# Kernel optimization log

Hardware: AMD Instinct MI355X
Metric: run time of the kernel (lower is better)

## Reference

```python
import jax, jax.numpy as jnp
import numpy as np

N = 50000      # num vertices
M = 10000      # num hyperedges
NNZ = 1600000  # incidence list length (avg degree 32)
D = 128        # in_features == out_features


def setup_inputs() -> dict:
    key = jax.random.key(0)
    k0, k1, k2, k3, k4, k5 = jax.random.split(key, 6)
    X = jax.random.normal(k0, (N, D), dtype=jnp.float32)
    X0 = jax.random.normal(k1, (N, D), dtype=jnp.float32)
    vertex = jax.random.randint(k2, (NNZ,), 0, N)
    edges = jax.random.randint(k3, (NNZ,), 0, M)
    # nn.Linear(D, D, bias=False) weight, kaiming-uniform-ish scale
    W = jax.random.uniform(k4, (D, D), dtype=jnp.float32,
                           minval=-1.0, maxval=1.0) / np.float32(np.sqrt(D))
    alpha = jax.random.uniform(k5, (), dtype=jnp.float32)
    beta = jnp.float32(0.5)
    return {"X": X, "X0": X0, "W": W, "alpha": alpha, "beta": beta,
            "vertex": vertex, "edges": edges}


def _scatter_mean(vals, idx, num_segments):
    # segment mean; empty segments -> 0 (matches torch_scatter 'mean')
    s = jax.ops.segment_sum(vals, idx, num_segments=num_segments)
    cnt = jax.ops.segment_sum(jnp.ones(idx.shape, vals.dtype), idx,
                              num_segments=num_segments)
    return s / jnp.maximum(cnt, 1.0)[:, None]


def reference(X, X0, W, alpha, beta, vertex, edges):
    Xve = X[vertex]                          # [NNZ, D] gather vertex -> incidence
    Xe = _scatter_mean(Xve, edges, M)        # [M, D]   hyperedge features
    Xev = Xe[edges]                          # [NNZ, D] gather edge -> incidence
    Xv = _scatter_mean(Xev, vertex, N)       # [N, D]   back to vertices
    Xi = (1.0 - alpha) * Xv + alpha * X0     # initial-residual mix
    return (1.0 - beta) * Xi + beta * (Xi @ W.T)  # identity-map mix + linear
```

## Files before the change

### kernel.cpp

```cpp
#include <hip/hip_runtime.h>
#include <hip/hip_bf16.h>


#define DD 128
#define NV 50000
#define ME 10000

#define CHUNK 4096
#define NEB 157
#define NVB 196
#define PB_CAP 12288

typedef __hip_bfloat16 bf16;
typedef __attribute__((ext_vector_type(8))) short short8v;
typedef __attribute__((ext_vector_type(4))) float float4v;

#define OFF_XE    0
#define OFF_ELIST 2560000
#define OFF_VLIST 8960000
#define OFF_EPAIR 15360000
#define OFF_VPAIR 21760000
#define OFF_XB    15360000
#define OFF_VOFF  28160000
#define OFF_EOFF  28360064
#define OFF_CBH   28400128
#define OFF_GBE   28401664
#define OFF_GBV   28402304
#define OFF_GCE   28403136
#define OFF_GCV   28403776
#define OFF_FLAG  28404608
#define OFF_WF    28404624
#define WS_USED   28470160

__device__ __forceinline__ float bf2f(unsigned short s) {
    union { unsigned u; float f; } x; x.u = ((unsigned)s) << 16; return x.f;
}
__device__ __forceinline__ unsigned f2bfu(float x) {
    union { bf16 h; unsigned short u; } c; c.h = __float2bfloat16(x); return (unsigned)c.u;
}
__device__ __forceinline__ float loadf(const void* p, long long i, unsigned f32) {
    if (f32) return ((const float*)p)[i];
    return bf2f(((const unsigned short*)p)[i]);
}
__device__ __forceinline__ float u2f_lo(unsigned x) {
    union { unsigned u; float f; } c; c.u = x << 16; return c.f;
}
__device__ __forceinline__ float u2f_hi(unsigned x) {
    union { unsigned u; float f; } c; c.u = x & 0xFFFF0000u; return c.f;
}
__device__ __forceinline__ void acc8(const uint4& u, float* a) {
    a[0] += u2f_lo(u.x); a[1] += u2f_hi(u.x);
    a[2] += u2f_lo(u.y); a[3] += u2f_hi(u.y);
    a[4] += u2f_lo(u.z); a[5] += u2f_hi(u.z);
    a[6] += u2f_lo(u.w); a[7] += u2f_hi(u.w);
}

__device__ __forceinline__ unsigned wave_is_fp32(const unsigned short* p) {
    int l = threadIdx.x & 63;
    int big = 0;
    for (int i = l; i < 256; i += 64) {
        unsigned e = (p[i] >> 7) & 0xFFu;
        if (e >= 0x90u) big++;
    }
    for (int s = 32; s > 0; s >>= 1) big += __shfl_down(big, s);
    return (__shfl(big, 0) >= 4) ? 1u : 0u;
}

__global__ __launch_bounds__(256) void prep_all(const void* X, const void* X0, const void* W,
                                                const void* beta_p,
                                                const int* __restrict__ vertex,
                                                const int* __restrict__ edges,
                                                unsigned* __restrict__ flags,
                                                unsigned short* __restrict__ Wfrag,
                                                unsigned* __restrict__ cbh, int nnz) {
    __shared__ unsigned h[NEB + NVB];
    int b = blockIdx.x, t = threadIdx.x;

    if (b == 0) {
        if (t < 64) {
            const unsigned short* px[3] = {(const unsigned short*)X,
                                           (const unsigned short*)X0,
                                           (const unsigned short*)W};
            for (int k = 0; k < 3; k++) {
                int big = 0;
                for (int i = t; i < 256; i += 64) {
                    unsigned e = (px[k][i] >> 7) & 0xFFu;
                    if (e >= 0x90u) big++;
                }
                for (int s = 32; s > 0; s >>= 1) big += __shfl_down(big, s);
                if (t == 0) flags[k] = (big >= 4) ? 1u : 0u;
            }
            if (t == 0) {
                unsigned short bb = *(const unsigned short*)beta_p;
                flags[3] = (bb == 0x3F00u) ? 0u : 1u;
            }
        }
        return;
    }

    if (b <= 8) {
        int blob = (b - 1) * 256 + t;
        unsigned fW = wave_is_fp32((const unsigned short*)W);
        unsigned short bu = *(const unsigned short*)beta_p;
        unsigned fS = (bu == 0x3F00u) ? 0u : 1u;
        int lane = blob & 63, kk = (blob >> 6) & 3, ct = blob >> 8;
        int nn = lane & 15, quad = lane >> 4;
        int c = ct * 16 + nn;
        int kbase = kk * 32 + quad * 8;
        float beta = loadf(beta_p, 0, fS);
        float omb = 1.f - beta;
        unsigned short hi[8], lo[8];
#pragma unroll
        for (int j = 0; j < 8; j++) {
            float wv = loadf(W, (long long)c * DD + kbase + j, fW);
            float v = beta * wv + ((kbase + j) == c ? omb : 0.f);
            unsigned short hh = (unsigned short)f2bfu(v);
            hi[j] = hh;
            lo[j] = (unsigned short)f2bfu(v - bf2f(hh));
        }
        uint4 ph, pl;
        ph.x = (unsigned)hi[0] | ((unsigned)hi[1] << 16);
        ph.y = (unsigned)hi[2] | ((unsigned)hi[3] << 16);
        ph.z = (unsigned)hi[4] | ((unsigned)hi[5] << 16);
        ph.w = (unsigned)hi[6] | ((unsigned)hi[7] << 16);
        pl.x = (unsigned)lo[0] | ((unsigned)lo[1] << 16);
        pl.y = (unsigned)lo[2] | ((unsigned)lo[3] << 16);
        pl.z = (unsigned)lo[4] | ((unsigned)lo[5] << 16);
        pl.w = (unsigned)lo[6] | ((unsigned)lo[7] << 16);
        ((uint4*)Wfrag)[blob] = ph;
        ((uint4*)Wfrag)[2048 + blob] = pl;
        return;
    }

    int hb = b - 9;
    for (int i = t; i < NEB + NVB; i += 256) h[i] = 0;
    __syncthreads();
    int stride = 512 * 256;
    for (int i = hb * 256 + t; i < nnz; i += stride) {
        atomicAdd(&h[edges[i] >> 6], 1u);
        atomicAdd(&h[NEB + (vertex[i] >> 8)], 1u);
    }
    __syncthreads();
    for (int i = t; i < NEB + NVB; i += 256) {
        unsigned v = h[i];
        if (v) atomicAdd(&cbh[i], v);
    }
}

__global__ __launch_bounds__(256) void conv_x(const void* __restrict__ X,
                                              unsigned short* __restrict__ Xb,
                                              const unsigned* __restrict__ flags) {
    if (!flags[0]) return;
    int i = blockIdx.x * 256 + threadIdx.x;
    if (i >= NV * DD / 8) return;
    const float4* p = (const float4*)X + (size_t)i * 2;
    float4 a = p[0], b = p[1];
    uint4 o;
    o.x = f2bfu(a.x) | (f2bfu(a.y) << 16);
    o.y = f2bfu(a.z) | (f2bfu(a.w) << 16);
    o.z = f2bfu(b.x) | (f2bfu(b.y) << 16);
    o.w = f2bfu(b.z) | (f2bfu(b.w) << 16);
    ((uint4*)Xb)[i] = o;
}

__global__ void scan353(const unsigned* __restrict__ cbh,
                        unsigned* __restrict__ gbe, unsigned* __restrict__ gbv,
                        unsigned* __restrict__ gce, unsigned* __restrict__ gcv,
                        unsigned* __restrict__ voff, unsigned* __restrict__ eoff,
                        int nnz) {
    __shared__ unsigned s[512];
    int t = threadIdx.x;
    unsigned v = (t < NEB + NVB) ? cbh[t] : 0u;
    s[t] = v;
    __syncthreads();
    for (int st = 1; st < 512; st <<= 1) {
        unsigned u = (t >= st) ? s[t - st] : 0u;
        __syncthreads();
        s[t] += u;
        __syncthreads();
    }
    unsigned excl = s[t] - v;
    if (t < NEB) {
        gbe[t] = excl; gce[t] = excl;
    } else if (t < NEB + NVB) {
        unsigned base = s[NEB - 1];
        gbv[t - NEB] = excl - base;
        gcv[t - NEB] = excl - base;
    }
    if (t == 0) {
        gbe[NEB] = (unsigned)nnz;
        gbv[NVB] = (unsigned)nnz;
        eoff[ME] = (unsigned)nnz;
        voff[NV] = (unsigned)nnz;
    }
}

__global__ __launch_bounds__(256) void build_pairs(const int* __restrict__ vertex,
                                                   const int* __restrict__ edges,
                                                   unsigned* __restrict__ gcur_e,
                                                   unsigned* __restrict__ gcur_v,
                                                   unsigned* __restrict__ epairs,
                                                   unsigned* __restrict__ vpairs, int nnz) {
    __shared__ unsigned buf[CHUNK];
    __shared__ unsigned hist[256], scn[256], loff[256], cur[256], gbase[256];
    int t = threadIdx.x;
    int base = blockIdx.x * CHUNK;
    int len = min(CHUNK, nnz - base);
    if (len <= 0) return;

    for (int phase = 0; phase < 2; phase++) {
        int sh = phase ? 8 : 6;
        int nb = phase ? NVB : NEB;
        unsigned* gcur = phase ? gcur_v : gcur_e;
        unsigned* pairs = phase ? vpairs : epairs;
        if (phase) __syncthreads();
        hist[t] = 0;
        __syncthreads();
        for (int i = t; i < len; i += 256) {
            int key = phase ? vertex[base + i] : edges[base + i];
            atomicAdd(&hist[key >> sh], 1u);
        }
        __syncthreads();
        unsigned hv = hist[t];
        scn[t] = hv;
        __syncthreads();
        for (int st = 1; st < 256; st <<= 1) {
            unsigned u = (t >= st) ? scn[t - st] : 0u;
            __syncthreads();
            scn[t] += u;
            __syncthreads();
        }
        loff[t] = scn[t] - hv;
        cur[t] = scn[t] - hv;
        if (t < nb && hv > 0) gbase[t] = atomicAdd(&gcur[t], hv);
        __syncthreads();
        for (int i = t; i < len; i += 256) {
            int k = phase ? vertex[base + i] : edges[base + i];
            int v2 = phase ? edges[base + i] : vertex[base + i];
            unsigned pk = ((unsigned)k << 16) | (unsigned)v2;
            unsigned p = atomicAdd(&cur[k >> sh], 1u);
            buf[p] = pk;
        }
        __syncthreads();
        for (int i = t; i < len; i += 256) {
            unsigned pk = buf[i];
            unsigned b = (pk >> 16) >> sh;
            pairs[gbase[b] + (i - loff[b])] = pk;
        }
    }
}

__global__ __launch_bounds__(256) void build_lists(const unsigned* __restrict__ epairs,
                                                   const unsigned* __restrict__ vpairs,
                                                   const unsigned* __restrict__ gbe,
                                                   const unsigned* __restrict__ gbv,
                                                   unsigned* __restrict__ eoff,
                                                   unsigned* __restrict__ voff,
                                                   unsigned* __restrict__ elist,
                                                   unsigned* __restrict__ vlist) {
    __shared__ unsigned buf[PB_CAP];
    __shared__ unsigned offs[256], curs[256];
    int b = blockIdx.x, t = threadIdx.x;
    const unsigned* pairs;
    unsigned* off;
    unsigned* list;
    unsigned s0, s1;
    int k0, nk;
    if (b < NEB) {
        pairs = epairs; off = eoff; list = elist;
        k0 = b << 6; nk = min(64, ME - k0);
        s0 = gbe[b]; s1 = gbe[b + 1];
    } else {
        int bb = b - NEB;
        pairs = vpairs; off = voff; list = vlist;
        k0 = bb << 8; nk = min(256, NV - k0);
        s0 = gbv[bb]; s1 = gbv[bb + 1];
    }
    int len = (int)(s1 - s0);

    curs[t] = 0;
    __syncthreads();
    for (int i = t; i < len; i += 256) {
        unsigned pk = pairs[s0 + i];
        atomicAdd(&curs[(pk >> 16) - k0], 1u);
    }
    __syncthreads();
    unsigned hv = curs[t];
    offs[t] = hv;
    __syncthreads();
    for (int st = 1; st < 256; st <<= 1) {
        unsigned u = (t >= st) ? offs[t - st] : 0u;
        __syncthreads();
        offs[t] += u;
        __syncthreads();
    }
    unsigned my_excl = offs[t] - hv;
    __syncthreads();
    offs[t] = my_excl;
    curs[t] = 0;
    if (t < nk) off[k0 + t] = s0 + my_excl;
    __syncthreads();

    if (len <= PB_CAP) {
        for (int i = t; i < len; i += 256) {
            unsigned pk = pairs[s0 + i];
            int lk = (int)(pk >> 16) - k0;
            unsigned p = offs[lk] + atomicAdd(&curs[lk], 1u);
            buf[p] = pk & 0xFFFFu;
        }
        __syncthreads();
        for (int i = t; i < len; i += 256) list[s0 + i] = buf[i];
    } else {
        for (int i = t; i < len; i += 256) {
            unsigned pk = pairs[s0 + i];
            int lk = (int)(pk >> 16) - k0;
            unsigned p = offs[lk] + atomicAdd(&curs[lk], 1u);
            list[s0 + p] = pk & 0xFFFFu;
        }
    }
}

__global__ __launch_bounds__(256, 8) void edge_agg(const void* __restrict__ X,
                                                   const unsigned short* __restrict__ Xb,
                                                   const unsigned* __restrict__ eoff,
                                                   const unsigned* __restrict__ elist,
                                                   unsigned short* __restrict__ Xe,
                                                   const unsigned* __restrict__ flags, int m) {
    __shared__ float red[4][DD];
    int e = blockIdx.x;
    int t = threadIdx.x, lane = t & 63, w = t >> 6;
    const unsigned short* Xp = flags[0] ? Xb : (const unsigned short*)X;
    unsigned s0 = eoff[e], s1 = eoff[e + 1];
    float a[8];
#pragma unroll
    for (int i = 0; i < 8; i++) a[i] = 0.f;

    int sub = t & 15;
    unsigned q = s0 + (unsigned)(t >> 4);
    for (; q + 48 < s1; q += 64) {
        unsigned v0 = elist[q], v1 = elist[q + 16];
        unsigned v2 = elist[q + 32], v3 = elist[q + 48];
        uint4 u0 = *(const uint4*)(Xp + (size_t)v0 * DD + 8 * sub);
        uint4 u1 = *(const uint4*)(Xp + (size_t)v1 * DD + 8 * sub);
        uint4 u2 = *(const uint4*)(Xp + (size_t)v2 * DD + 8 * sub);
        uint4 u3 = *(const uint4*)(Xp + (size_t)v3 * DD + 8 * sub);
        acc8(u0, a); acc8(u1, a); acc8(u2, a); acc8(u3, a);
    }
    for (; q + 16 < s1; q += 32) {
        unsigned v0 = elist[q], v1 = elist[q + 16];
        uint4 u0 = *(const uint4*)(Xp + (size_t)v0 * DD + 8 * sub);
        uint4 u1 = *(const uint4*)(Xp + (size_t)v1 * DD + 8 * sub);
        acc8(u0, a); acc8(u1, a);
    }
    if (q < s1) {
        unsigned v0 = elist[q];
        uint4 u0 = *(const uint4*)(Xp + (size_t)v0 * DD + 8 * sub);
        acc8(u0, a);
    }
#pragma unroll
    for (int i = 0; i < 8; i++) {
        a[i] += __shfl_xor(a[i], 16);
        a[i] += __shfl_xor(a[i], 32);
    }
    if ((lane >> 4) == 0) {
#pragma unroll
        for (int i = 0; i < 8; i++) red[w][8 * sub + i] = a[i];
    }
    __syncthreads();
    if (t < DD) {
        float inv = (s1 > s0) ? 1.f / (float)(s1 - s0) : 1.f;
        float v = (red[0][t] + red[1][t] + red[2][t] + red[3][t]) * inv;
        Xe[(size_t)e * DD + t] = (unsigned short)f2bfu(v);
    }
}

__global__ __launch_bounds__(512, 6) void vertex_out(const unsigned short* __restrict__ Xe,
                                                     const unsigned* __restrict__ voff,
                                                     const unsigned* __restrict__ vlist,
                                                     const void* __restrict__ X0,
                                                     const unsigned short* __restrict__ Wfrag,
                                                     const void* __restrict__ alpha_p,
                                                     void* __restrict__ out,
                                                     const unsigned* __restrict__ flags, int n) {
    __shared__ short8v A_hi[544];
    __shared__ short8v A_lo[544];
    int t = threadIdx.x, lane = t & 63, w = t >> 6;
    unsigned fX = flags[0], f0 = flags[1], fS = flags[3];
    float alpha = loadf(alpha_p, 0, fS);
    float oma = 1.f - alpha;
    int v0 = blockIdx.x * 32;

    int g = lane >> 4, sub = lane & 15;
    for (int j = 0; j < 4; j++) {
        int r = w * 4 + j, v = v0 + r;
        int rt = r >> 4, mm = r & 15;
        int idx = (rt * 4 + (sub >> 2)) * 68 + (sub & 3) * 17 + mm;
        float a[8];
#pragma unroll
        for (int i = 0; i < 8; i++) a[i] = 0.f;
        if (v < n) {
            unsigned s0 = voff[v], s1 = voff[v + 1];
            unsigned q = s0;
            for (; q + 8 <= s1; q += 8) {
                unsigned e0 = vlist[q + g];
                unsigned e1 = vlist[q + 4 + g];
                uint4 u0 = *(const uint4*)(Xe + (size_t)e0 * DD + 8 * sub);
                uint4 u1 = *(const uint4*)(Xe + (size_t)e1 * DD + 8 * sub);
                acc8(u0, a); acc8(u1, a);
            }
            if (q + 4 <= s1) {
                unsigned e0 = vlist[q + g];
                uint4 u0 = *(const uint4*)(Xe + (size_t)e0 * DD + 8 * sub);
                acc8(u0, a);
                q += 4;
            }
            int rem = (int)(s1 - q);
            if (g < rem) {
                unsigned e0 = vlist[q + g];
                uint4 u0 = *(const uint4*)(Xe + (size_t)e0 * DD + 8 * sub);
                acc8(u0, a);
            }
#pragma unroll
            for (int i = 0; i < 8; i++) {
                a[i] += __shfl_xor(a[i], 16);
                a[i] += __shfl_xor(a[i], 32);
            }
            if (g == 0) {
                float inv = (s1 > s0) ? 1.f / (float)(s1 - s0) : 1.f;
                float x0[8];
                if (!f0) {
                    uint4 xu = *(const uint4*)((const unsigned short*)X0 + (size_t)v * DD + 8 * sub);
                    x0[0] = u2f_lo(xu.x); x0[1] = u2f_hi(xu.x);
                    x0[2] = u2f_lo(xu.y); x0[3] = u2f_hi(xu.y);
                    x0[4] = u2f_lo(xu.z); x0[5] = u2f_hi(xu.z);
                    x0[6] = u2f_lo(xu.w); x0[7] = u2f_hi(xu.w);
                } else {
                    const float4* p = (const float4*)((const float*)X0 + (size_t)v * DD + 8 * sub);
                    float4 xA = p[0], xB = p[1];
                    x0[0] = xA.x; x0[1] = xA.y; x0[2] = xA.z; x0[3] = xA.w;
                    x0[4] = xB.x; x0[5] = xB.y; x0[6] = xB.z; x0[7] = xB.w;
                }
                short8v ah, al;
#pragma unroll
                for (int i = 0; i < 8; i++) {
                    float xi = oma * (a[i] * inv) + alpha * x0[i];
                    unsigned short hh = (unsigned short)f2bfu(xi);
                    ah[i] = (short)hh;
                    al[i] = (short)f2bfu(xi - bf2f(hh));
                }
                A_hi[idx] = ah;
                A_lo[idx] = al;
            }
        } else if (g == 0) {
            short8v zf = {0, 0, 0, 0, 0, 0, 0, 0};
            A_hi[idx] = zf;
            A_lo[idx] = zf;
        }
    }

    __syncthreads();
    int rt = w & 1, ct = w >> 1;
    short8v ah[4], al[4];
#pragma unroll
    for (int kk = 0; kk < 4; kk++) {
        int ridx = (rt * 4 + kk) * 68 + (lane >> 4) * 17 + (lane & 15);
        ah[kk] = A_hi[ridx];
        al[kk] = A_lo[ridx];
    }
    const short8v* Bh = (const short8v*)Wfrag;
    const short8v* Bl = Bh + 2048;
#pragma unroll
    for (int tt = 0; tt < 2; tt++) {
        int c2 = ct + 4 * tt;
        float4v acc = {0.f, 0.f, 0.f, 0.f};
#pragma unroll
        for (int kk = 0; kk < 4; kk++) {
            short8v bh = Bh[(c2 * 4 + kk) * 64 + lane];
            short8v bl = Bl[(c2 * 4 + kk) * 64 + lane];
            acc = __builtin_amdgcn_mfma_f32_16x16x32_bf16(ah[kk], bh, acc, 0, 0, 0);
            acc = __builtin_amdgcn_mfma_f32_16x16x32_bf16(al[kk], bh, acc, 0, 0, 0);
            acc = __builtin_amdgcn_mfma_f32_16x16x32_bf16(ah[kk], bl, acc, 0, 0, 0);
        }
        int col = c2 * 16 + (lane & 15);
        int rbase = v0 + rt * 16 + (lane >> 4) * 4;
#pragma unroll
        for (int reg = 0; reg < 4; reg++) {
            int row = rbase + reg;
            if (row < n) {
                if (fX) ((float*)out)[(size_t)row * DD + col] = acc[reg];
                else    ((bf16*)out)[(size_t)row * DD + col] = __float2bfloat16(acc[reg]);
            }
        }
    }
}

extern "C" void kernel_launch(void* const* d_in, const int* in_sizes, int n_in,
                              void* d_out, int out_size, void* d_ws, size_t ws_size,
                              hipStream_t stream) {
    const void* X      = d_in[0];
    const void* X0     = d_in[1];
    const void* W      = d_in[2];
    const void* alpha  = d_in[3];
    const void* beta   = d_in[4];
    const int*  vertex = (const int*)d_in[5];
    const int*  edges  = (const int*)d_in[6];
    const int nnz = in_sizes[5];

    char* ws = (char*)d_ws;
    unsigned short* Xe = (unsigned short*)(ws + OFF_XE);
    unsigned* elist  = (unsigned*)(ws + OFF_ELIST);
    unsigned* vlist  = (unsigned*)(ws + OFF_VLIST);
    unsigned* epairs = (unsigned*)(ws + OFF_EPAIR);
    unsigned* vpairs = (unsigned*)(ws + OFF_VPAIR);
    unsigned short* Xb = (unsigned short*)(ws + OFF_XB);
    unsigned* voff   = (unsigned*)(ws + OFF_VOFF);
    unsigned* eoff   = (unsigned*)(ws + OFF_EOFF);
    unsigned* cbh    = (unsigned*)(ws + OFF_CBH);
    unsigned* gbe    = (unsigned*)(ws + OFF_GBE);
    unsigned* gbv    = (unsigned*)(ws + OFF_GBV);
    unsigned* gce    = (unsigned*)(ws + OFF_GCE);
    unsigned* gcv    = (unsigned*)(ws + OFF_GCV);
    unsigned* flags  = (unsigned*)(ws + OFF_FLAG);
    unsigned short* Wfrag = (unsigned short*)(ws + OFF_WF);

    hipMemsetAsync(ws + OFF_CBH, 0, 1536, stream);

    prep_all<<<521, 256, 0, stream>>>(X, X0, W, beta, vertex, edges,
                                      flags, Wfrag, cbh, nnz);

    scan353<<<1, 512, 0, stream>>>(cbh, gbe, gbv, gce, gcv, voff, eoff, nnz);

    int pa_blocks = (nnz + CHUNK - 1) / CHUNK;
    build_pairs<<<pa_blocks, 256, 0, stream>>>(vertex, edges, gce, gcv,
                                               epairs, vpairs, nnz);

    build_lists<<<NEB + NVB, 256, 0, stream>>>(epairs, vpairs, gbe, gbv,
                                               eoff, voff, elist, vlist);

    conv_x<<<(NV * DD / 8 + 255) / 256, 256, 0, stream>>>(X, Xb, flags);

    edge_agg<<<ME, 256, 0, stream>>>(X, Xb, eoff, elist, Xe, flags, ME);

    vertex_out<<<(NV + 31) / 32, 512, 0, stream>>>(Xe, voff, vlist, X0, Wfrag,
                                                   alpha, d_out, flags, NV);
}
```

Baseline: 269.6 us.

## Reuse edge-sorted buffer for vertex bucketing and shrink vertex_out blocks to 16 rows

build_pairs now reads vertex/edges once into registers and builds the vertex-keyed pass by swapping halves of the edge-sorted packed pairs already held in shared memory. This removes the second global read of the index arrays. vertex_out drops from 32 rows and 512 threads per block to 16 rows and 256 threads, with four waves each covering two column tiles. The smaller blocks give finer scheduling granularity and a smaller LDS footprint, at the cost of loading W fragments from global twice as often per output row.

```diff
diff --git a/kernel.cpp b/kernel.cpp
--- a/kernel.cpp
+++ b/kernel.cpp
@@ -208,45 +208,92 @@
     int len = min(CHUNK, nnz - base);
     if (len <= 0) return;
 
-    for (int phase = 0; phase < 2; phase++) {
-        int sh = phase ? 8 : 6;
-        int nb = phase ? NVB : NEB;
-        unsigned* gcur = phase ? gcur_v : gcur_e;
-        unsigned* pairs = phase ? vpairs : epairs;
-        if (phase) __syncthreads();
-        hist[t] = 0;
-        __syncthreads();
-        for (int i = t; i < len; i += 256) {
-            int key = phase ? vertex[base + i] : edges[base + i];
-            atomicAdd(&hist[key >> sh], 1u);
-        }
-        __syncthreads();
-        unsigned hv = hist[t];
-        scn[t] = hv;
-        __syncthreads();
-        for (int st = 1; st < 256; st <<= 1) {
-            unsigned u = (t >= st) ? scn[t - st] : 0u;
-            __syncthreads();
-            scn[t] += u;
-            __syncthreads();
-        }
-        loff[t] = scn[t] - hv;
-        cur[t] = scn[t] - hv;
-        if (t < nb && hv > 0) gbase[t] = atomicAdd(&gcur[t], hv);
-        __syncthreads();
-        for (int i = t; i < len; i += 256) {
-            int k = phase ? vertex[base + i] : edges[base + i];
-            int v2 = phase ? edges[base + i] : vertex[base + i];
-            unsigned pk = ((unsigned)k << 16) | (unsigned)v2;
-            unsigned p = atomicAdd(&cur[k >> sh], 1u);
+    unsigned pkr[16];
+
+    hist[t] = 0;
+    __syncthreads();
+#pragma unroll
+    for (int it = 0; it < 16; it++) {
+        int i = t + it * 256;
+        if (i < len) {
+            unsigned e = (unsigned)edges[base + i];
+            unsigned v = (unsigned)vertex[base + i];
+            unsigned pk = (e << 16) | v;
+            pkr[it] = pk;
+            atomicAdd(&hist[pk >> 22], 1u);
+        }
+    }
+    __syncthreads();
+    unsigned hv = hist[t];
+    scn[t] = hv;
+    __syncthreads();
+    for (int st = 1; st < 256; st <<= 1) {
+        unsigned u = (t >= st) ? scn[t - st] : 0u;
+        __syncthreads();
+        scn[t] += u;
+        __syncthreads();
+    }
+    loff[t] = scn[t] - hv;
+    cur[t] = scn[t] - hv;
+    if (t < NEB && hv > 0) gbase[t] = atomicAdd(&gcur_e[t], hv);
+    __syncthreads();
+#pragma unroll
+    for (int it = 0; it < 16; it++) {
+        int i = t + it * 256;
+        if (i < len) {
+            unsigned pk = pkr[it];
+            unsigned p = atomicAdd(&cur[pk >> 22], 1u);
             buf[p] = pk;
         }
-        __syncthreads();
-        for (int i = t; i < len; i += 256) {
+    }
+    __syncthreads();
+    for (int i = t; i < len; i += 256) {
+        unsigned pk = buf[i];
+        unsigned b = pk >> 22;
+        epairs[gbase[b] + (i - loff[b])] = pk;
+    }
+
+    __syncthreads();
+    hist[t] = 0;
+    __syncthreads();
+#pragma unroll
+    for (int it = 0; it < 16; it++) {
+        int i = t + it * 256;
+        if (i < len) {
             unsigned pk = buf[i];
-            unsigned b = (pk >> 16) >> sh;
-            pairs[gbase[b] + (i - loff[b])] = pk;
-        }
+            unsigned npk = (pk << 16) | (pk >> 16);
+            pkr[it] = npk;
+            atomicAdd(&hist[npk >> 24], 1u);
+        }
+    }
+    __syncthreads();
+    hv = hist[t];
+    scn[t] = hv;
+    __syncthreads();
+    for (int st = 1; st < 256; st <<= 1) {
+        unsigned u = (t >= st) ? scn[t - st] : 0u;
+        __syncthreads();
+        scn[t] += u;
+        __syncthreads();
+    }
+    loff[t] = scn[t] - hv;
+    cur[t] = scn[t] - hv;
+    if (t < NVB && hv > 0) gbase[t] = atomicAdd(&gcur_v[t], hv);
+    __syncthreads();
+#pragma unroll
+    for (int it = 0; it < 16; it++) {
+        int i = t + it * 256;
+        if (i < len) {
+            unsigned npk = pkr[it];
+            unsigned p = atomicAdd(&cur[npk >> 24], 1u);
+            buf[p] = npk;
+        }
+    }
+    __syncthreads();
+    for (int i = t; i < len; i += 256) {
+        unsigned npk = buf[i];
+        unsigned b = npk >> 24;
+        vpairs[gbase[b] + (i - loff[b])] = npk;
     }
 }
 
@@ -374,7 +421,7 @@
     }
 }
 
-__global__ __launch_bounds__(512, 6) void vertex_out(const unsigned short* __restrict__ Xe,
+__global__ __launch_bounds__(256, 8) void vertex_out(const unsigned short* __restrict__ Xe,
                                                      const unsigned* __restrict__ voff,
                                                      const unsigned* __restrict__ vlist,
                                                      const void* __restrict__ X0,
@@ -382,19 +429,18 @@
                                                      const void* __restrict__ alpha_p,
                                                      void* __restrict__ out,
                                                      const unsigned* __restrict__ flags, int n) {
-    __shared__ short8v A_hi[544];
-    __shared__ short8v A_lo[544];
+    __shared__ short8v A_hi[272];
+    __shared__ short8v A_lo[272];
     int t = threadIdx.x, lane = t & 63, w = t >> 6;
     unsigned fX = flags[0], f0 = flags[1], fS = flags[3];
     float alpha = loadf(alpha_p, 0, fS);
     float oma = 1.f - alpha;
-    int v0 = blockIdx.x * 32;
+    int v0 = blockIdx.x * 16;
 
     int g = lane >> 4, sub = lane & 15;
     for (int j = 0; j < 4; j++) {
         int r = w * 4 + j, v = v0 + r;
-        int rt = r >> 4, mm = r & 15;
-        int idx = (rt * 4 + (sub >> 2)) * 68 + (sub & 3) * 17 + mm;
+        int idx = (sub >> 2) * 68 + (sub & 3) * 17 + r;
         float a[8];
 #pragma unroll
         for (int i = 0; i < 8; i++) a[i] = 0.f;
@@ -459,11 +505,11 @@
     }
 
     __syncthreads();
-    int rt = w & 1, ct = w >> 1;
+    int ct = w;
     short8v ah[4], al[4];
 #pragma unroll
     for (int kk = 0; kk < 4; kk++) {
-        int ridx = (rt * 4 + kk) * 68 + (lane >> 4) * 17 + (lane & 15);
+        int ridx = kk * 68 + (lane >> 4) * 17 + (lane & 15);
         ah[kk] = A_hi[ridx];
         al[kk] = A_lo[ridx];
     }
@@ -482,7 +528,7 @@
             acc = __builtin_amdgcn_mfma_f32_16x16x32_bf16(ah[kk], bl, acc, 0, 0, 0);
         }
         int col = c2 * 16 + (lane & 15);
-        int rbase = v0 + rt * 16 + (lane >> 4) * 4;
+        int rbase = v0 + (lane >> 4) * 4;
 #pragma unroll
         for (int reg = 0; reg < 4; reg++) {
             int row = rbase + reg;
@@ -541,6 +587,6 @@
 
     edge_agg<<<ME, 256, 0, stream>>>(X, Xb, eoff, elist, Xe, flags, ME);
 
-    vertex_out<<<(NV + 31) / 32, 512, 0, stream>>>(Xe, voff, vlist, X0, Wfrag,
+    vertex_out<<<(NV + 15) / 16, 256, 0, stream>>>(Xe, voff, vlist, X0, Wfrag,
                                                    alpha, d_out, flags, NV);
 }
```

After: 265.0 us. No clear change (-1.7%).
